# Performance work log

Hardware: AMD Instinct MI355X
Metric: run time of the kernel (lower is better)

## Reference

```python
import jax, jax.numpy as jnp
import numpy as np

B, N, K, V = 16, 256, 2048, 768

def setup_inputs() -> dict:
    key = jax.random.key(0)
    k1, k2 = jax.random.split(key)
    inputs = jax.random.normal(k1, (B, N, V), dtype=jnp.float32)
    prototypes = jax.random.normal(k2, (K, V), dtype=jnp.float32)
    return {"inputs": inputs, "prototypes": prototypes}

def reference(inputs, prototypes):
    # distances[b,n,k] = sum_v (inputs[b,n,v] - prototypes[k,v])**2
    x_sq = jnp.sum(inputs * inputs, axis=-1, keepdims=True)          # [B,N,1]
    p_sq = jnp.sum(prototypes * prototypes, axis=-1)                  # [K]
    xp = jnp.einsum("bnv,kv->bnk", inputs, prototypes)               # [B,N,K]
    distances = x_sq + p_sq[None, None, :] - 2.0 * xp
    return (distances, prototypes)
```

## Files before the change

kernel.cpp:

```cpp
#include <hip/hip_runtime.h>
#include <hip/hip_bf16.h>
#include <stdint.h>

#define Kdim 2048
#define Vdim 768
#define Mdim 4096

#define BM 256
#define BN 128
#define BK 128
#define NT (Vdim / BK)

typedef __attribute__((ext_vector_type(4))) int  i32x4;
typedef __attribute__((ext_vector_type(16))) int i32x16;

#define CFENCE asm volatile("" ::: "memory")

__device__ __forceinline__ void gld_lds16(const void* g, void* l) {
    __builtin_amdgcn_global_load_lds((const __attribute__((address_space(1))) void*)g,
                                     (__attribute__((address_space(3))) void*)l, 16, 0, 0);
}

__global__ __launch_bounds__(256) void rowquant(const float* __restrict__ x,
                                                const float* __restrict__ p,
                                                int8_t* __restrict__ Aq,
                                                int8_t* __restrict__ Pq,
                                                float* __restrict__ xsq,
                                                float* __restrict__ psq,
                                                float* __restrict__ sxa,
                                                float* __restrict__ spa,
                                                float* __restrict__ proto_out) {
    const int row = blockIdx.x * 4 + (threadIdx.x >> 6);
    const int lane = threadIdx.x & 63;

    const float* src;
    int8_t* dq;
    float *sq, *sc, *cpy = nullptr;
    if (row < Mdim) {
        src = x + (size_t)row * Vdim; dq = Aq + (size_t)row * Vdim;
        sq = xsq + row; sc = sxa + row;
    } else {
        const int r = row - Mdim;
        src = p + (size_t)r * Vdim; dq = Pq + (size_t)r * Vdim;
        sq = psq + r; sc = spa + r; cpy = proto_out + (size_t)r * Vdim;
    }

    float4 v[3];
    float s = 0.f, mx = 0.f;
#pragma unroll
    for (int j = 0; j < 3; ++j) {
        v[j] = *reinterpret_cast<const float4*>(src + j * 256 + lane * 4);
        s += v[j].x * v[j].x + v[j].y * v[j].y + v[j].z * v[j].z + v[j].w * v[j].w;
        mx = fmaxf(mx, fmaxf(fmaxf(fabsf(v[j].x), fabsf(v[j].y)),
                             fmaxf(fabsf(v[j].z), fabsf(v[j].w))));
        if (cpy) *reinterpret_cast<float4*>(cpy + j * 256 + lane * 4) = v[j];
    }
#pragma unroll
    for (int off = 32; off > 0; off >>= 1) {
        s += __shfl_xor(s, off);
        mx = fmaxf(mx, __shfl_xor(mx, off));
    }
    mx = fmaxf(mx, 1e-20f);
    const float inv = 127.0f / mx;
#pragma unroll
    for (int j = 0; j < 3; ++j) {
        int q0 = min(127, max(-127, __float2int_rn(v[j].x * inv)));
        int q1 = min(127, max(-127, __float2int_rn(v[j].y * inv)));
        int q2 = min(127, max(-127, __float2int_rn(v[j].z * inv)));
        int q3 = min(127, max(-127, __float2int_rn(v[j].w * inv)));
        int packed = (q0 & 0xff) | ((q1 & 0xff) << 8) | ((q2 & 0xff) << 16) | (q3 << 24);
        *reinterpret_cast<int*>(dq + j * 256 + lane * 4) = packed;
    }
    if (lane == 0) { *sq = s; *sc = mx * (1.0f / 127.0f); }
}

__global__ __launch_bounds__(512) void gemm_dist_i8(const int8_t* __restrict__ Aq,
                                                    const int8_t* __restrict__ Pq,
                                                    const float* __restrict__ xsq,
                                                    const float* __restrict__ psq,
                                                    const float* __restrict__ sxa,
                                                    const float* __restrict__ spa,
                                                    float* __restrict__ out) {
    __shared__ int8_t As[3][BM * BK];
    __shared__ int8_t Bs[3][BN * BK];

    const int t = threadIdx.x;
    const int lane = t & 63;
    const int wave = t >> 6;
    const int wr = wave >> 1;
    const int wc = wave & 1;
    const int ln31 = lane & 31;
    const int lh = lane >> 5;

    const int wg = (blockIdx.x & 7) * 32 + (blockIdx.x >> 3);
    const int bm = wg >> 4, bn = wg & 15;
    const int m0 = bm * BM, n0 = bn * BN;

    const int srow = t >> 3;
    const int scol = ((t & 7) ^ (srow & 7)) * 16;
    const int8_t* Ag = Aq + (size_t)(m0 + srow) * Vdim + scol;
    const int8_t* Bg = Pq + (size_t)(n0 + srow) * Vdim + scol;
    const int ldsw = wave * 1024;

    int offA[2][4], offB[2][4];
#pragma unroll
    for (int mt = 0; mt < 2; ++mt)
#pragma unroll
        for (int ks = 0; ks < 4; ++ks) {
            const int k16 = ks * 2 + lh;
            const int rA = wr * 64 + mt * 32 + ln31;
            const int rB = wc * 64 + mt * 32 + ln31;
            offA[mt][ks] = rA * BK + ((k16 ^ (rA & 7)) * 16);
            offB[mt][ks] = rB * BK + ((k16 ^ (rB & 7)) * 16);
        }

    i32x16 acc[2][2] = {};

    auto stgA = [&](int buf, int kt, int q) {
        gld_lds16(Ag + (size_t)q * 64 * Vdim + kt * BK, (void*)(&As[buf][q * 8192 + ldsw]));
    };
    auto stgB = [&](int buf, int kt, int q) {
        gld_lds16(Bg + (size_t)q * 64 * Vdim + kt * BK, (void*)(&Bs[buf][q * 8192 + ldsw]));
    };

#pragma unroll
    for (int pb = 0; pb < 3; ++pb) {
        stgA(pb, pb, 0); stgA(pb, pb, 1); stgA(pb, pb, 2); stgA(pb, pb, 3);
        stgB(pb, pb, 0); stgB(pb, pb, 1);
    }
    asm volatile("s_waitcnt vmcnt(12)" ::: "memory");
    __builtin_amdgcn_s_barrier();
    CFENCE;

    int cb = 0, cs = 2;
    for (int kt = 0; kt < NT; ++kt) {
        const int8_t* Ap = &As[cb][0];
        const int8_t* Bp = &Bs[cb][0];
        const bool doStage = (kt >= 1 && kt <= NT - 3);

        i32x4 bq[2][4], a0[4];
#pragma unroll
        for (int nt = 0; nt < 2; ++nt)
#pragma unroll
            for (int ks = 0; ks < 4; ++ks)
                bq[nt][ks] = *reinterpret_cast<const i32x4*>(Bp + offB[nt][ks]);
#pragma unroll
        for (int ks = 0; ks < 4; ++ks)
            a0[ks] = *reinterpret_cast<const i32x4*>(Ap + offA[0][ks]);
        if (doStage) { stgA(cs, kt + 2, 0); stgA(cs, kt + 2, 1); stgA(cs, kt + 2, 2); }
        CFENCE;
        __builtin_amdgcn_s_barrier();
        CFENCE;
        __builtin_amdgcn_s_setprio(1);
#pragma unroll
        for (int ks = 0; ks < 4; ++ks)
#pragma unroll
            for (int nt = 0; nt < 2; ++nt)
                acc[0][nt] = __builtin_amdgcn_mfma_i32_32x32x32_i8(a0[ks], bq[nt][ks], acc[0][nt], 0, 0, 0);
        __builtin_amdgcn_s_setprio(0);
        CFENCE;
        __builtin_amdgcn_s_barrier();
        CFENCE;

        i32x4 a1[4];
#pragma unroll
        for (int ks = 0; ks < 4; ++ks)
            a1[ks] = *reinterpret_cast<const i32x4*>(Ap + offA[1][ks]);
        if (doStage) { stgA(cs, kt + 2, 3); stgB(cs, kt + 2, 0); stgB(cs, kt + 2, 1); }
        CFENCE;
        __builtin_amdgcn_s_barrier();
        CFENCE;
        __builtin_amdgcn_s_setprio(1);
#pragma unroll
        for (int ks = 0; ks < 4; ++ks)
#pragma unroll
            for (int nt = 0; nt < 2; ++nt)
                acc[1][nt] = __builtin_amdgcn_mfma_i32_32x32x32_i8(a1[ks], bq[nt][ks], acc[1][nt], 0, 0, 0);
        __builtin_amdgcn_s_setprio(0);
        CFENCE;
        if (kt <= NT - 3)      asm volatile("s_waitcnt vmcnt(6)" ::: "memory");
        else if (kt == NT - 2) asm volatile("s_waitcnt vmcnt(0)" ::: "memory");
        __builtin_amdgcn_s_barrier();
        CFENCE;

        cb = (cb == 2) ? 0 : cb + 1;
        cs = (cs == 2) ? 0 : cs + 1;
    }

    float ps_[2], sp_[2];
    int col_[2];
#pragma unroll
    for (int nt = 0; nt < 2; ++nt) {
        col_[nt] = n0 + wc * 64 + nt * 32 + ln31;
        ps_[nt] = psq[col_[nt]];
        sp_[nt] = spa[col_[nt]];
    }
#pragma unroll
    for (int mt = 0; mt < 2; ++mt)
#pragma unroll
        for (int reg = 0; reg < 16; ++reg) {
            const int row = m0 + wr * 64 + mt * 32 + (reg & 3) + 8 * (reg >> 2) + 4 * lh;
            const float xs = xsq[row];
            const float m2sx = -2.0f * sxa[row];
#pragma unroll
            for (int nt = 0; nt < 2; ++nt)
                out[(size_t)row * Kdim + col_[nt]] =
                    xs + ps_[nt] + m2sx * sp_[nt] * (float)acc[mt][nt][reg];
        }
}

extern "C" void kernel_launch(void* const* d_in, const int* in_sizes, int n_in,
                              void* d_out, int out_size, void* d_ws, size_t ws_size,
                              hipStream_t stream) {
    const float* x = (const float*)d_in[0];
    const float* p = (const float*)d_in[1];
    float* out = (float*)d_out;

    char* ws = (char*)d_ws;
    int8_t* Aq = (int8_t*)ws;
    int8_t* Pq = (int8_t*)(ws + 3145728);
    float* xsq = (float*)(ws + 4718592);
    float* psq = (float*)(ws + 4734976);
    float* sxa = (float*)(ws + 4743168);
    float* spa = (float*)(ws + 4759552);

    rowquant<<<(Mdim + Kdim) / 4, 256, 0, stream>>>(x, p, Aq, Pq, xsq, psq, sxa, spa,
                                                    out + (size_t)Mdim * Kdim);
    gemm_dist_i8<<<(Mdim / BM) * (Kdim / BN), 512, 0, stream>>>(Aq, Pq, xsq, psq, sxa, spa, out);
}
```

Baseline: 27.86 us.

## Shrink GEMM tile to 128x128 with double buffering and two blocks per CU

The int8 GEMM tile shrinks from 256x128 with 512 threads and a triple-buffered, split-phase pipeline to a 128x128 tile with 256 threads. It now uses simple double buffering and launch bounds that allow two blocks per CU. Each iteration prefetches the next K-slice, loads all A/B fragments, issues all MFMAs, then waits on vmcnt(0) and one barrier. The aim is more blocks and occupancy to hide latency with a simpler schedule. The cost is less data reuse per block, more global and L2 traffic, and a full memory wait every iteration.

```diff
diff --git a/kernel.cpp b/kernel.cpp
--- a/kernel.cpp
+++ b/kernel.cpp
@@ -6,10 +6,10 @@
 #define Vdim 768
 #define Mdim 4096
 
-#define BM 256
-#define BN 128
-#define BK 128
-#define NT (Vdim / BK)
+#define BMx 128
+#define BNx 128
+#define BKx 128
+#define NTx (Vdim / BKx)
 
 typedef __attribute__((ext_vector_type(4))) int  i32x4;
 typedef __attribute__((ext_vector_type(16))) int i32x16;
@@ -74,15 +74,15 @@
     if (lane == 0) { *sq = s; *sc = mx * (1.0f / 127.0f); }
 }
 
-__global__ __launch_bounds__(512) void gemm_dist_i8(const int8_t* __restrict__ Aq,
-                                                    const int8_t* __restrict__ Pq,
-                                                    const float* __restrict__ xsq,
-                                                    const float* __restrict__ psq,
-                                                    const float* __restrict__ sxa,
-                                                    const float* __restrict__ spa,
-                                                    float* __restrict__ out) {
-    __shared__ int8_t As[3][BM * BK];
-    __shared__ int8_t Bs[3][BN * BK];
+__global__ __launch_bounds__(256, 2) void gemm_dist_i8(const int8_t* __restrict__ Aq,
+                                                       const int8_t* __restrict__ Pq,
+                                                       const float* __restrict__ xsq,
+                                                       const float* __restrict__ psq,
+                                                       const float* __restrict__ sxa,
+                                                       const float* __restrict__ spa,
+                                                       float* __restrict__ out) {
+    __shared__ int8_t As[2][BMx * BKx];
+    __shared__ int8_t Bs[2][BNx * BKx];
 
     const int t = threadIdx.x;
     const int lane = t & 63;
@@ -92,15 +92,16 @@
     const int ln31 = lane & 31;
     const int lh = lane >> 5;
 
-    const int wg = (blockIdx.x & 7) * 32 + (blockIdx.x >> 3);
-    const int bm = wg >> 4, bn = wg & 15;
-    const int m0 = bm * BM, n0 = bn * BN;
+    const int wg = (blockIdx.x & 7) * 64 + (blockIdx.x >> 3);
+    const int bm = wg >> 4;
+    const int bn = wg & 15;
+    const int m0 = bm * BMx, n0 = bn * BNx;
 
     const int srow = t >> 3;
     const int scol = ((t & 7) ^ (srow & 7)) * 16;
     const int8_t* Ag = Aq + (size_t)(m0 + srow) * Vdim + scol;
     const int8_t* Bg = Pq + (size_t)(n0 + srow) * Vdim + scol;
-    const int ldsw = wave * 1024;
+    const int ldsoff = wave * 1024;
 
     int offA[2][4], offB[2][4];
 #pragma unroll
@@ -110,81 +111,55 @@
             const int k16 = ks * 2 + lh;
             const int rA = wr * 64 + mt * 32 + ln31;
             const int rB = wc * 64 + mt * 32 + ln31;
-            offA[mt][ks] = rA * BK + ((k16 ^ (rA & 7)) * 16);
-            offB[mt][ks] = rB * BK + ((k16 ^ (rB & 7)) * 16);
+            offA[mt][ks] = rA * BKx + ((k16 ^ (rA & 7)) * 16);
+            offB[mt][ks] = rB * BKx + ((k16 ^ (rB & 7)) * 16);
         }
 
+    auto stage = [&](int buf, int kt) {
+#pragma unroll
+        for (int q = 0; q < 4; ++q)
+            gld_lds16(Ag + (size_t)q * 32 * Vdim + kt * BKx, (void*)(&As[buf][q * 4096 + ldsoff]));
+#pragma unroll
+        for (int q = 0; q < 4; ++q)
+            gld_lds16(Bg + (size_t)q * 32 * Vdim + kt * BKx, (void*)(&Bs[buf][q * 4096 + ldsoff]));
+    };
+
     i32x16 acc[2][2] = {};
 
-    auto stgA = [&](int buf, int kt, int q) {
-        gld_lds16(Ag + (size_t)q * 64 * Vdim + kt * BK, (void*)(&As[buf][q * 8192 + ldsw]));
-    };
-    auto stgB = [&](int buf, int kt, int q) {
-        gld_lds16(Bg + (size_t)q * 64 * Vdim + kt * BK, (void*)(&Bs[buf][q * 8192 + ldsw]));
-    };
-
-#pragma unroll
-    for (int pb = 0; pb < 3; ++pb) {
-        stgA(pb, pb, 0); stgA(pb, pb, 1); stgA(pb, pb, 2); stgA(pb, pb, 3);
-        stgB(pb, pb, 0); stgB(pb, pb, 1);
-    }
-    asm volatile("s_waitcnt vmcnt(12)" ::: "memory");
+    stage(0, 0);
+    asm volatile("s_waitcnt vmcnt(0)" ::: "memory");
     __builtin_amdgcn_s_barrier();
     CFENCE;
 
-    int cb = 0, cs = 2;
-    for (int kt = 0; kt < NT; ++kt) {
-        const int8_t* Ap = &As[cb][0];
-        const int8_t* Bp = &Bs[cb][0];
-        const bool doStage = (kt >= 1 && kt <= NT - 3);
-
-        i32x4 bq[2][4], a0[4];
-#pragma unroll
-        for (int nt = 0; nt < 2; ++nt)
-#pragma unroll
-            for (int ks = 0; ks < 4; ++ks)
-                bq[nt][ks] = *reinterpret_cast<const i32x4*>(Bp + offB[nt][ks]);
+    int cur = 0;
+    for (int kt = 0; kt < NTx; ++kt) {
+        if (kt + 1 < NTx) stage(cur ^ 1, kt + 1);
+
+        const int8_t* Ap = &As[cur][0];
+        const int8_t* Bp = &Bs[cur][0];
+        i32x4 af[2][4], bf[2][4];
+#pragma unroll
+        for (int mt = 0; mt < 2; ++mt)
+#pragma unroll
+            for (int ks = 0; ks < 4; ++ks) {
+                af[mt][ks] = *reinterpret_cast<const i32x4*>(Ap + offA[mt][ks]);
+                bf[mt][ks] = *reinterpret_cast<const i32x4*>(Bp + offB[mt][ks]);
+            }
+        CFENCE;
+        __builtin_amdgcn_s_setprio(1);
 #pragma unroll
         for (int ks = 0; ks < 4; ++ks)
-            a0[ks] = *reinterpret_cast<const i32x4*>(Ap + offA[0][ks]);
-        if (doStage) { stgA(cs, kt + 2, 0); stgA(cs, kt + 2, 1); stgA(cs, kt + 2, 2); }
+#pragma unroll
+            for (int mt = 0; mt < 2; ++mt)
+#pragma unroll
+                for (int nt = 0; nt < 2; ++nt)
+                    acc[mt][nt] = __builtin_amdgcn_mfma_i32_32x32x32_i8(af[mt][ks], bf[nt][ks], acc[mt][nt], 0, 0, 0);
+        __builtin_amdgcn_s_setprio(0);
         CFENCE;
+        asm volatile("s_waitcnt vmcnt(0)" ::: "memory");
         __builtin_amdgcn_s_barrier();
         CFENCE;
-        __builtin_amdgcn_s_setprio(1);
-#pragma unroll
-        for (int ks = 0; ks < 4; ++ks)
-#pragma unroll
-            for (int nt = 0; nt < 2; ++nt)
-                acc[0][nt] = __builtin_amdgcn_mfma_i32_32x32x32_i8(a0[ks], bq[nt][ks], acc[0][nt], 0, 0, 0);
-        __builtin_amdgcn_s_setprio(0);
-        CFENCE;
-        __builtin_amdgcn_s_barrier();
-        CFENCE;
-
-        i32x4 a1[4];
-#pragma unroll
-        for (int ks = 0; ks < 4; ++ks)
-            a1[ks] = *reinterpret_cast<const i32x4*>(Ap + offA[1][ks]);
-        if (doStage) { stgA(cs, kt + 2, 3); stgB(cs, kt + 2, 0); stgB(cs, kt + 2, 1); }
-        CFENCE;
-        __builtin_amdgcn_s_barrier();
-        CFENCE;
-        __builtin_amdgcn_s_setprio(1);
-#pragma unroll
-        for (int ks = 0; ks < 4; ++ks)
-#pragma unroll
-            for (int nt = 0; nt < 2; ++nt)
-                acc[1][nt] = __builtin_amdgcn_mfma_i32_32x32x32_i8(a1[ks], bq[nt][ks], acc[1][nt], 0, 0, 0);
-        __builtin_amdgcn_s_setprio(0);
-        CFENCE;
-        if (kt <= NT - 3)      asm volatile("s_waitcnt vmcnt(6)" ::: "memory");
-        else if (kt == NT - 2) asm volatile("s_waitcnt vmcnt(0)" ::: "memory");
-        __builtin_amdgcn_s_barrier();
-        CFENCE;
-
-        cb = (cb == 2) ? 0 : cb + 1;
-        cs = (cs == 2) ? 0 : cs + 1;
+        cur ^= 1;
     }
 
     float ps_[2], sp_[2];
@@ -226,5 +201,5 @@
 
     rowquant<<<(Mdim + Kdim) / 4, 256, 0, stream>>>(x, p, Aq, Pq, xsq, psq, sxa, spa,
                                                     out + (size_t)Mdim * Kdim);
-    gemm_dist_i8<<<(Mdim / BM) * (Kdim / BN), 512, 0, stream>>>(Aq, Pq, xsq, psq, sxa, spa, out);
-}
+    gemm_dist_i8<<<(Mdim / BMx) * (Kdim / BNx), 256, 0, stream>>>(Aq, Pq, xsq, psq, sxa, spa, out);
+}
```

Result: slower. 29.94 us (+7.5%).
